# Performance work log

Measured on AMD Instinct MI355X. Metric: run time of the kernel, lower is better.

## Reference

```python
import jax, jax.numpy as jnp
import numpy as np

VAR_FLOOR = 0.002
BS, A, IN, H, L, NNH, ATT, NACT = 1024, 32, 96, 64, 16, 64, 32, 16


def _lin(x, w, b):
    return x @ w.T + b


def _lrelu(x):
    return jax.nn.leaky_relu(x, 0.01)


def setup_inputs() -> dict:
    key = jax.random.key(0)
    ks = jax.random.split(key, 24)
    def w(k, o, i):
        return jax.random.normal(k, (o, i), jnp.float32) / np.float32(np.sqrt(i))
    def b(k, o):
        return jax.random.normal(k, (o,), jnp.float32) * 0.01
    N = BS * A
    return {
        "inputs": jax.random.normal(ks[0], (N, IN), jnp.float32),
        "hidden_state": jax.random.normal(ks[1], (N, H), jnp.float32),
        "eps": jax.random.normal(ks[2], (N, A * L), jnp.float32),
        "fc1_w": w(ks[3], H, IN), "fc1_b": b(ks[4], H),
        "gru_wih": w(ks[5], 3 * H, H), "gru_whh": w(ks[6], 3 * H, H),
        "gru_bih": b(ks[7], 3 * H), "gru_bhh": b(ks[8], 3 * H),
        "fc2_w": w(ks[9], NACT, H), "fc2_b": b(ks[10], NACT),
        "emb_w1": w(ks[11], NNH, H), "emb_b1": b(ks[12], NNH),
        "bn_g": jnp.ones((NNH,), jnp.float32), "bn_b": jnp.zeros((NNH,), jnp.float32),
        "emb_w2": w(ks[13], A * L * 2, NNH), "emb_b2": b(ks[14], A * L * 2),
        "msg_w1": w(ks[15], NNH, H + L), "msg_b1": b(ks[16], NNH),
        "msg_w2": w(ks[17], NACT, NNH), "msg_b2": b(ks[18], NACT),
        "wq_w": w(ks[19], ATT, H), "wq_b": b(ks[20], ATT),
        "wk_w": w(ks[21], ATT, L), "wk_b": b(ks[22], ATT),
        "bs": BS, "t": 0,
    }


def reference(inputs, hidden_state, eps, fc1_w, fc1_b, gru_wih, gru_whh, gru_bih,
              gru_bhh, fc2_w, fc2_b, emb_w1, emb_b1, bn_g, bn_b, emb_w2, emb_b2,
              msg_w1, msg_b1, msg_w2, msg_b2, wq_w, wq_b, wk_w, wk_b, bs, t):
    Hd = fc1_w.shape[0]
    x = jax.nn.relu(_lin(inputs, fc1_w, fc1_b))
    h_in = hidden_state.reshape(-1, Hd)
    # GRUCell
    gi = _lin(x, gru_wih, gru_bih)
    gh = _lin(h_in, gru_whh, gru_bhh)
    ir, iz, inn = jnp.split(gi, 3, axis=-1)
    hr, hz, hn = jnp.split(gh, 3, axis=-1)
    r = jax.nn.sigmoid(ir + hr)
    z = jax.nn.sigmoid(iz + hz)
    n = jnp.tanh(inn + r * hn)
    h = (1.0 - z) * n + z * h_in
    q = _lin(h, fc2_w, fc2_b)
    # embed_net: Linear -> BatchNorm(train) -> LeakyReLU -> Linear
    z1 = _lin(h, emb_w1, emb_b1)
    z1 = bn_g * (z1 - z1.mean(0)) / jnp.sqrt(z1.var(0) + 1e-5) + bn_b
    lat_par = _lin(_lrelu(z1), emb_w2, emb_b2)
    D = lat_par.shape[-1] // 2
    Ld = wk_w.shape[1]
    Ag = D // Ld
    mu = lat_par[:, :D]
    var = jnp.clip(jnp.exp(lat_par[:, D:]), VAR_FLOOR, None)
    latent = (mu + jnp.sqrt(var) * eps).reshape(bs, Ag, Ag, Ld)  # [b,i,j,L]
    # msg_net on (h of receiver j, latent[b,i,j])
    h3 = h.reshape(bs, Ag, Hd)
    h_rep = jnp.broadcast_to(h3[:, None, :, :], (bs, Ag, Ag, Hd))  # [b,i,j]=h[b,j]
    msg_in = jnp.concatenate([h_rep, latent], axis=-1)
    msg = _lin(_lrelu(_lin(msg_in, msg_w1, msg_b1)), msg_w2, msg_b2)  # (b,A,A,n_act)
    # attention gating
    att = wq_w.shape[0]
    query = _lin(h, wq_w, wq_b).reshape(bs, Ag, att) / np.float32(np.sqrt(att))
    key_ = _lin(latent, wk_w, wk_b)  # (b,A,A,att)
    alpha = jnp.einsum('bia,bija->bij', query, key_)
    alpha = jnp.where(jnp.eye(Ag, dtype=bool)[None], -1e9, alpha)
    alpha = jax.nn.softmax(alpha, axis=-1)
    agg = jnp.einsum('bij,bijn->bjn', alpha, msg)  # sum gated msgs over sender i
    return_q = q + agg.reshape(bs * Ag, -1)
    return (return_q, h)
```

## Files before the change

kernel.cpp:

```cpp
#include <hip/hip_runtime.h>
#include <math.h>

namespace {

constexpr int NROW = 32768;
constexpr int HDIM = 64;
constexpr int DH   = 512;

typedef __attribute__((ext_vector_type(8))) short bf16x8;
typedef __attribute__((ext_vector_type(4))) float f32x4;
typedef __attribute__((ext_vector_type(4))) unsigned uint4e;
typedef __attribute__((ext_vector_type(2))) unsigned uint2e;

__device__ __forceinline__ float sigmoidf_(float x) { return 1.f / (1.f + __expf(-x)); }
__device__ __forceinline__ float lrelu_(float x) { return x > 0.f ? x : 0.01f * x; }
__device__ __forceinline__ unsigned pkbf(float a, float b) {
  unsigned ua = __float_as_uint(a) + 0x8000u;
  unsigned ub = __float_as_uint(b) + 0x8000u;
  return __builtin_amdgcn_perm(ub, ua, 0x07060302);
}

__global__ __launch_bounds__(512, 1) void k_fgru(
    const float* __restrict__ in,
    const float* __restrict__ hprev,
    const float* __restrict__ fc1w, const float* __restrict__ fc1b,
    const float* __restrict__ wih, const float* __restrict__ whh,
    const float* __restrict__ bih, const float* __restrict__ bhh,
    float* __restrict__ hT, float* __restrict__ hout) {
  __shared__ char smem[73728];
  const int t = threadIdx.x;
  const int n0 = blockIdx.x * 128;
  short*    xS = (short*)smem;
  unsigned* gU = (unsigned*)(smem + 18432);
  float*    trF = (float*)(smem + 18432);

  const float2* wih2 = (const float2*)wih;
  const float2* whh2 = (const float2*)whh;
  {
    float2 wv[12];
#pragma unroll
    for (int i = 0; i < 12; ++i) {
      int idx = t + 512 * i;
      int row = idx >> 5, kp = idx & 31;
      wv[i] = wih2[row * 32 + kp];
    }
#pragma unroll
    for (int i = 0; i < 12; ++i) {
      int idx = t + 512 * i;
      int row = idx >> 5, kp = idx & 31;
      int gate = row >> 6, cl = row & 63;
      gU[(gate * 64 + cl) * 36 + kp] = pkbf(wv[i].x, wv[i].y);
    }
#pragma unroll
    for (int i = 0; i < 12; ++i) {
      int idx = t + 512 * i;
      int row = idx >> 5, kp = idx & 31;
      wv[i] = whh2[row * 32 + kp];
    }
#pragma unroll
    for (int i = 0; i < 12; ++i) {
      int idx = t + 512 * i;
      int row = idx >> 5, kp = idx & 31;
      int gate = row >> 6, cl = row & 63;
      gU[((gate + 3) * 64 + cl) * 36 + kp] = pkbf(wv[i].x, wv[i].y);
    }
  }

  const int w = t >> 6, l = t & 63;
  const int m = l & 15, g = l >> 4;
  const int rowA = n0 + w * 16 + m;

  bf16x8 af[3];
#pragma unroll
  for (int ks = 0; ks < 3; ++ks) {
    const float4* p = (const float4*)(in + (size_t)rowA * 96 + ks * 32 + g * 8);
    float4 a = p[0], b = p[1];
    union { unsigned u[4]; bf16x8 h; } tw;
    tw.u[0] = pkbf(a.x, a.y); tw.u[1] = pkbf(a.z, a.w);
    tw.u[2] = pkbf(b.x, b.y); tw.u[3] = pkbf(b.z, b.w);
    af[ks] = tw.h;
  }
  {
    f32x4 accx[4];
#pragma unroll
    for (int ct = 0; ct < 4; ++ct) accx[ct] = (f32x4){0.f, 0.f, 0.f, 0.f};
#pragma unroll
    for (int ct = 0; ct < 4; ++ct)
#pragma unroll
      for (int ks = 0; ks < 3; ++ks) {
        const float4* p = (const float4*)(fc1w + (ct * 16 + m) * 96 + ks * 32 + g * 8);
        float4 a = p[0], b = p[1];
        union { unsigned u[4]; bf16x8 h; } tw;
        tw.u[0] = pkbf(a.x, a.y); tw.u[1] = pkbf(a.z, a.w);
        tw.u[2] = pkbf(b.x, b.y); tw.u[3] = pkbf(b.z, b.w);
        accx[ct] = __builtin_amdgcn_mfma_f32_16x16x32_bf16(af[ks], tw.h, accx[ct], 0, 0, 0);
      }
#pragma unroll
    for (int ct = 0; ct < 4; ++ct) {
      int c = ct * 16 + m;
      float bc = fc1b[c];
#pragma unroll
      for (int reg = 0; reg < 4; ++reg) {
        int nl = w * 16 + g * 4 + reg;
        float v = fmaxf(accx[ct][reg] + bc, 0.f);
        xS[nl * 72 + c] = (short)((__float_as_uint(v) + 0x8000u) >> 16);
      }
    }
  }
  __syncthreads();

  bf16x8 ax[2], ah[2];
#pragma unroll
  for (int ks = 0; ks < 2; ++ks) {
    ax[ks] = *(const bf16x8*)(xS + (w * 16 + m) * 72 + ks * 32 + g * 8);
    const float4* p = (const float4*)(hprev + (size_t)rowA * 64 + ks * 32 + g * 8);
    float4 a = p[0], b = p[1];
    union { unsigned u[4]; bf16x8 h; } tw;
    tw.u[0] = pkbf(a.x, a.y); tw.u[1] = pkbf(a.z, a.w);
    tw.u[2] = pkbf(b.x, b.y); tw.u[3] = pkbf(b.z, b.w);
    ah[ks] = tw.h;
  }
  const short* gS = (const short*)gU;
  float hc[4][4];
#pragma unroll 1
  for (int ct = 0; ct < 4; ++ct) {
    f32x4 a_ir = (f32x4){0.f,0.f,0.f,0.f}, a_iz = (f32x4){0.f,0.f,0.f,0.f},
          a_in = (f32x4){0.f,0.f,0.f,0.f}, a_hr = (f32x4){0.f,0.f,0.f,0.f},
          a_hz = (f32x4){0.f,0.f,0.f,0.f}, a_hn = (f32x4){0.f,0.f,0.f,0.f};
    int crow = ct * 16 + m;
#pragma unroll
    for (int ks = 0; ks < 2; ++ks) {
      bf16x8 b0 = *(const bf16x8*)(gS + (0 * 64 + crow) * 72 + ks * 32 + g * 8);
      bf16x8 b1 = *(const bf16x8*)(gS + (1 * 64 + crow) * 72 + ks * 32 + g * 8);
      bf16x8 b2 = *(const bf16x8*)(gS + (2 * 64 + crow) * 72 + ks * 32 + g * 8);
      bf16x8 b3 = *(const bf16x8*)(gS + (3 * 64 + crow) * 72 + ks * 32 + g * 8);
      bf16x8 b4 = *(const bf16x8*)(gS + (4 * 64 + crow) * 72 + ks * 32 + g * 8);
      bf16x8 b5 = *(const bf16x8*)(gS + (5 * 64 + crow) * 72 + ks * 32 + g * 8);
      a_ir = __builtin_amdgcn_mfma_f32_16x16x32_bf16(ax[ks], b0, a_ir, 0, 0, 0);
      a_iz = __builtin_amdgcn_mfma_f32_16x16x32_bf16(ax[ks], b1, a_iz, 0, 0, 0);
      a_in = __builtin_amdgcn_mfma_f32_16x16x32_bf16(ax[ks], b2, a_in, 0, 0, 0);
      a_hr = __builtin_amdgcn_mfma_f32_16x16x32_bf16(ah[ks], b3, a_hr, 0, 0, 0);
      a_hz = __builtin_amdgcn_mfma_f32_16x16x32_bf16(ah[ks], b4, a_hz, 0, 0, 0);
      a_hn = __builtin_amdgcn_mfma_f32_16x16x32_bf16(ah[ks], b5, a_hn, 0, 0, 0);
    }
    float bir = bih[crow], biz = bih[64 + crow], bin = bih[128 + crow];
    float bhr = bhh[crow], bhz = bhh[64 + crow], bhn = bhh[128 + crow];
#pragma unroll
    for (int reg = 0; reg < 4; ++reg) {
      int nl = w * 16 + g * 4 + reg;
      float hv = hprev[(size_t)(n0 + nl) * 64 + crow];
      float r  = sigmoidf_(a_ir[reg] + bir + a_hr[reg] + bhr);
      float z  = sigmoidf_(a_iz[reg] + biz + a_hz[reg] + bhz);
      float nn = tanhf(a_in[reg] + bin + r * (a_hn[reg] + bhn));
      hc[ct][reg] = (1.f - z) * nn + z * hv;
    }
  }
  __syncthreads();
#pragma unroll
  for (int ct = 0; ct < 4; ++ct)
#pragma unroll
    for (int reg = 0; reg < 4; ++reg)
      trF[(ct * 16 + m) * 133 + w * 16 + g * 4 + reg] = hc[ct][reg];
  __syncthreads();
#pragma unroll
  for (int i = 0; i < 16; ++i) {
    int idx = t + 512 * i;
    int nl = idx & 127, cl = idx >> 7;
    hT[(size_t)cl * NROW + n0 + nl] = trF[cl * 133 + nl];
  }
#pragma unroll
  for (int i = 0; i < 16; ++i) {
    int idx = t + 512 * i;
    int c = idx & 63, nl = idx >> 6;
    hout[(size_t)(n0 + nl) * 64 + c] = trF[c * 133 + nl];
  }
}

__global__ __launch_bounds__(256) void k_heads(const float* __restrict__ hT,
    const float* __restrict__ fc2w, const float* __restrict__ fc2b,
    const float* __restrict__ wqw, const float* __restrict__ wkw,
    const float* __restrict__ ew1, const float* __restrict__ eb1,
    float* __restrict__ qT, float* __restrict__ qkT, float* __restrict__ z1T,
    float* __restrict__ part) {
  __shared__ char smem[36864];
  const int t = threadIdx.x;
  const int n0 = blockIdx.x * 128;
  unsigned* hU = (unsigned*)smem;
  unsigned* wU = (unsigned*)(smem + 18432);
  float* sp1 = (float*)(smem + 18432 + 13824);
  float* sp2 = sp1 + 256;
  const float qs = 0.17677669529663687f;

  {
    float va[16], vb[16];
#pragma unroll
    for (int i = 0; i < 16; ++i) {
      int idx = t + 256 * i;
      int nl = idx & 127, kp = idx >> 7;
      va[i] = hT[(size_t)(2 * kp) * NROW + n0 + nl];
      vb[i] = hT[(size_t)(2 * kp + 1) * NROW + n0 + nl];
    }
#pragma unroll
    for (int i = 0; i < 16; ++i) {
      int idx = t + 256 * i;
      int nl = idx & 127, kp = idx >> 7;
      hU[nl * 36 + kp] = pkbf(va[i], vb[i]);
    }
  }
  {
    float2 wv[10];
#pragma unroll
    for (int i = 0; i < 10; ++i) {
      int idx = t + 256 * i;
      int kp = idx & 31, cl = idx >> 5;
      const float* src = (cl < 16) ? (fc2w + cl * 64) : (ew1 + (cl - 16) * 64);
      wv[i] = *(const float2*)(src + 2 * kp);
    }
#pragma unroll
    for (int i = 0; i < 10; ++i) {
      int idx = t + 256 * i;
      int kp = idx & 31, cl = idx >> 5;
      int dst = (cl < 16) ? cl : (cl + 16);
      wU[dst * 36 + kp] = pkbf(wv[i].x, wv[i].y);
    }
  }
  {
    int kp = t & 31, ll = t >> 5;
#pragma unroll
    for (int h = 0; h < 2; ++h) {
      int row = ll + 8 * h;
      float s0 = 0.f, s1 = 0.f;
#pragma unroll
      for (int a = 0; a < 32; ++a) {
        float wk = wkw[a * 16 + row];
        s0 = fmaf(wk, wqw[a * 64 + 2 * kp], s0);
        s1 = fmaf(wk, wqw[a * 64 + 2 * kp + 1], s1);
      }
      wU[(16 + row) * 36 + kp] = pkbf(s0 * qs, s1 * qs);
    }
  }
  __syncthreads();

  const int w = t >> 6, l = t & 63;
  const int m = l & 15, g = l >> 4;
  const short* sH = (const short*)hU;
  const short* sW = (const short*)wU;

  bf16x8 af[2][2];
#pragma unroll
  for (int mt = 0; mt < 2; ++mt)
#pragma unroll
    for (int ks = 0; ks < 2; ++ks)
      af[mt][ks] = *(const bf16x8*)(sH + (w * 32 + mt * 16 + m) * 72 + ks * 32 + g * 8);

  f32x4 acc[2][6];
#pragma unroll
  for (int mt = 0; mt < 2; ++mt)
#pragma unroll
    for (int ct = 0; ct < 6; ++ct) acc[mt][ct] = (f32x4){0.f, 0.f, 0.f, 0.f};
#pragma unroll
  for (int ct = 0; ct < 6; ++ct)
#pragma unroll
    for (int ks = 0; ks < 2; ++ks) {
      bf16x8 bw = *(const bf16x8*)(sW + (ct * 16 + m) * 72 + ks * 32 + g * 8);
#pragma unroll
      for (int mt = 0; mt < 2; ++mt)
        acc[mt][ct] = __builtin_amdgcn_mfma_f32_16x16x32_bf16(af[mt][ks], bw, acc[mt][ct], 0, 0, 0);
    }

  float s1[4], s2[4];
#pragma unroll
  for (int zt = 0; zt < 4; ++zt) { s1[zt] = 0.f; s2[zt] = 0.f; }
#pragma unroll
  for (int mt = 0; mt < 2; ++mt) {
    int nb = n0 + w * 32 + mt * 16 + g * 4;
    {
      float bc = fc2b[m];
      f32x4 v;
#pragma unroll
      for (int reg = 0; reg < 4; ++reg) v[reg] = acc[mt][0][reg] + bc;
      *(f32x4*)(qT + (size_t)m * NROW + nb) = v;
    }
    *(f32x4*)(qkT + (size_t)m * NROW + nb) = acc[mt][1];
#pragma unroll
    for (int ct = 2; ct < 6; ++ct) {
      int z = (ct - 2) * 16 + m;
      float bc = eb1[z];
      f32x4 v;
#pragma unroll
      for (int reg = 0; reg < 4; ++reg) {
        float zv = acc[mt][ct][reg] + bc;
        v[reg] = zv;
        s1[ct - 2] += zv;
        s2[ct - 2] = fmaf(zv, zv, s2[ct - 2]);
      }
      *(f32x4*)(z1T + (size_t)z * NROW + nb) = v;
    }
  }
#pragma unroll
  for (int zt = 0; zt < 4; ++zt) {
    s1[zt] += __shfl_down(s1[zt], 16, 64);
    s1[zt] += __shfl_down(s1[zt], 32, 64);
    s2[zt] += __shfl_down(s2[zt], 16, 64);
    s2[zt] += __shfl_down(s2[zt], 32, 64);
  }
  if (l < 16) {
#pragma unroll
    for (int zt = 0; zt < 4; ++zt) {
      sp1[w * 64 + zt * 16 + m] = s1[zt];
      sp2[w * 64 + zt * 16 + m] = s2[zt];
    }
  }
  __syncthreads();
  if (t < 64) {
    float a1 = sp1[t] + sp1[64 + t] + sp1[128 + t] + sp1[192 + t];
    float a2 = sp2[t] + sp2[64 + t] + sp2[128 + t] + sp2[192 + t];
    part[(size_t)blockIdx.x * 128 + t] = a1;
    part[(size_t)blockIdx.x * 128 + 64 + t] = a2;
  }
}

__global__ void k_bnstat(const float* __restrict__ part,
    const float* __restrict__ bng, const float* __restrict__ bnb,
    float* __restrict__ stat) {
  int c = threadIdx.x;
  float s1 = 0.f, s2 = 0.f;
  for (int b = 0; b < 256; ++b) {
    s1 += part[(size_t)b * 128 + c];
    s2 += part[(size_t)b * 128 + 64 + c];
  }
  float mean = s1 * (1.f / NROW);
  float var = s2 * (1.f / NROW) - mean * mean;
  float rstd = rsqrtf(var + 1e-5f);
  float sc = bng[c] * rstd;
  stat[c] = sc;
  stat[64 + c] = bnb[c] - mean * sc;
}

__global__ __launch_bounds__(512, 1) void k_emb_gemm(const float* __restrict__ z1T,
    const float* __restrict__ stat,
    const float* __restrict__ ew2, const float* __restrict__ eb2,
    const float* __restrict__ eps,
    unsigned* __restrict__ latB16g) {
  __shared__ char smem[161280];
  const int t = threadIdx.x;
  const int n0 = blockIdx.x * 128;
  unsigned* aU = (unsigned*)smem;
  unsigned* wU = (unsigned*)(smem + 17920);

  const int w = t >> 6, l = t & 63;
  const int m = l & 15, g = l >> 4;
  const float2* ew2_2 = (const float2*)ew2;
  const float stdfloor = 0.04472135955f;

  {
    float va[8], vb[8];
#pragma unroll
    for (int i = 0; i < 8; ++i) {
      int idx = t + 512 * i;
      int nl = idx & 127, kp = idx >> 7;
      va[i] = z1T[(size_t)(2 * kp) * NROW + n0 + nl];
      vb[i] = z1T[(size_t)(2 * kp + 1) * NROW + n0 + nl];
    }
#pragma unroll
    for (int i = 0; i < 8; ++i) {
      int idx = t + 512 * i;
      int nl = idx & 127, kp = idx >> 7;
      float v0 = lrelu_(fmaf(stat[2 * kp], va[i], stat[64 + 2 * kp]));
      float v1 = lrelu_(fmaf(stat[2 * kp + 1], vb[i], stat[64 + 2 * kp + 1]));
      aU[nl * 35 + kp] = pkbf(v0, v1);
    }
  }
#pragma unroll 1
  for (int rb = 0; rb < 4; ++rb) {
    float2 wv[16];
#pragma unroll
    for (int j = 0; j < 16; ++j) {
      int idx = t + 512 * (rb * 16 + j);
      int kp = idx & 31, r = idx >> 5;
      wv[j] = ew2_2[(size_t)r * 32 + kp];
    }
#pragma unroll
    for (int j = 0; j < 16; ++j) {
      int idx = t + 512 * (rb * 16 + j);
      int kp = idx & 31, r = idx >> 5;
      int chunk = (r >> 6) & 7;
      int lrow = (r & 63) + ((r >> 9) << 6);
      wU[chunk * 4480 + lrow * 35 + kp] = pkbf(wv[j].x, wv[j].y);
    }
  }
  float epsC[16];
#pragma unroll
  for (int ct = 0; ct < 4; ++ct)
#pragma unroll
    for (int reg = 0; reg < 4; ++reg)
      epsC[ct * 4 + reg] =
          eps[(size_t)(n0 + w * 16 + g * 4 + reg) * 512 + ct * 16 + m];
  __syncthreads();

  const short* sA = (const short*)aU;
  bf16x8 af[2];
#pragma unroll
  for (int ks = 0; ks < 2; ++ks)
    af[ks] = *(const bf16x8*)(sA + (w * 16 + m) * 70 + ks * 32 + g * 8);

  const int rowG = n0 + w * 16 + g * 4;

#pragma unroll 1
  for (int cb = 0; cb < 8; ++cb) {
    const int c0 = cb * 64;
    float epsN[16];
    if (cb < 7) {
#pragma unroll
      for (int ct = 0; ct < 4; ++ct)
#pragma unroll
        for (int reg = 0; reg < 4; ++reg)
          epsN[ct * 4 + reg] =
              eps[(size_t)(rowG + reg) * 512 + c0 + 64 + ct * 16 + m];
    }

    const short* sW = (const short*)(wU + cb * 4480);
    f32x4 accm[4], accl[4];
#pragma unroll
    for (int ct = 0; ct < 4; ++ct) {
      accm[ct] = (f32x4){0.f, 0.f, 0.f, 0.f};
      accl[ct] = (f32x4){0.f, 0.f, 0.f, 0.f};
    }
#pragma unroll
    for (int ct = 0; ct < 4; ++ct)
#pragma unroll
      for (int ks = 0; ks < 2; ++ks) {
        bf16x8 bm = *(const bf16x8*)(sW + (ct * 16 + m) * 70 + ks * 32 + g * 8);
        bf16x8 bl = *(const bf16x8*)(sW + (64 + ct * 16 + m) * 70 + ks * 32 + g * 8);
        accm[ct] = __builtin_amdgcn_mfma_f32_16x16x32_bf16(af[ks], bm, accm[ct], 0, 0, 0);
        accl[ct] = __builtin_amdgcn_mfma_f32_16x16x32_bf16(af[ks], bl, accl[ct], 0, 0, 0);
      }

#pragma unroll
    for (int ct = 0; ct < 4; ++ct) {
      int c = c0 + ct * 16 + m;
      float ebm = eb2[c], ebl = eb2[DH + c];
#pragma unroll
      for (int reg = 0; reg < 4; ++reg) {
        float mu = accm[ct][reg] + ebm;
        float lv = accl[ct][reg] + ebl;
        float sd = fmaxf(__expf(0.5f * lv), stdfloor);
        float lat = fmaf(sd, epsC[ct * 4 + reg], mu);
        float lat2 = __shfl_xor(lat, 1, 64);
        if (!(m & 1)) {
          latB16g[(size_t)(rowG + reg) * 256 + (c0 >> 1) + ct * 8 + (m >> 1)] =
              pkbf(lat, lat2);
        }
      }
    }
#pragma unroll
    for (int i2 = 0; i2 < 16; ++i2) epsC[i2] = epsN[i2];
  }
}

constexpr int LATB_OFF = 0;
constexpr int H3B_OFF  = 40960;
constexpr int W1H_OFF  = 45568;
constexpr int W1L_OFF  = 54784;
constexpr int W2P_OFF  = 57344;
constexpr int ALL_OFF  = 59648;
constexpr int MT_OFF   = 63872;
constexpr int QKL_OFF  = 74112;
__global__ __launch_bounds__(256, 1) void k_msg(
    const unsigned* __restrict__ latB16g, const float* __restrict__ qkT,
    const float* __restrict__ qT, const float* __restrict__ hrow,
    const float* __restrict__ w1, const float* __restrict__ b1,
    const float* __restrict__ w2, const float* __restrict__ b2,
    float* __restrict__ out) {
  __shared__ char smem[76672];
  const int t = threadIdx.x;
  const int b = blockIdx.x;
  const int b32 = b * 32;
  unsigned* latB_dw = (unsigned*)(smem + LATB_OFF);

  {
    const uint4e* g4 = (const uint4e*)latB16g + (size_t)b32 * 64;
#pragma unroll
    for (int half = 0; half < 2; ++half) {
      uint4e v[4];
#pragma unroll
      for (int it = 0; it < 4; ++it) v[it] = g4[t + 256 * (4 * half + it)];
#pragma unroll
      for (int it = 0; it < 4; ++it) {
        int idx = t + 256 * (4 * half + it);
        int i = idx >> 6;
        int rem = idx & 63;
        int j = rem >> 1, hh = rem & 1;
        unsigned* dst = latB_dw + (i * 32 + j) * 10 + hh * 4;
        *(uint2e*)dst = (uint2e){v[it].x, v[it].y};
        *(uint2e*)(dst + 2) = (uint2e){v[it].z, v[it].w};
      }
    }
  }
  {
    float* qkL = (float*)(smem + QKL_OFF);
    int i = t & 31;
    float v0 = qkT[(size_t)((t >> 5)) * NROW + b32 + i];
    float v1 = qkT[(size_t)((t >> 5) + 8) * NROW + b32 + i];
    qkL[i * 20 + (t >> 5)] = v0;
    qkL[i * 20 + (t >> 5) + 8] = v1;
  }
  {
    int cp = t & 31, jj = t >> 5;
    const float2* h2 = (const float2*)hrow;
    float2 hv[4];
#pragma unroll
    for (int it = 0; it < 4; ++it)
      hv[it] = h2[((size_t)(b32 + jj + 8 * it) * 64 + 2 * cp) >> 1];
    unsigned* dst = (unsigned*)(smem + H3B_OFF);
#pragma unroll
    for (int it = 0; it < 4; ++it)
      dst[(jj + 8 * it) * 36 + cp] = pkbf(hv[it].x, hv[it].y);
  }
  {
    int kp = t & 31, cc = t >> 5;
    const float2* w12 = (const float2*)w1;
    float2 wv[8];
#pragma unroll
    for (int it = 0; it < 8; ++it)
      wv[it] = w12[((cc + 8 * it) * 80 + 2 * kp) >> 1];
    unsigned* dst = (unsigned*)(smem + W1H_OFF);
#pragma unroll
    for (int it = 0; it < 8; ++it)
      dst[(cc + 8 * it) * 36 + kp] = pkbf(wv[it].x, wv[it].y);
  }
  {
    int lp = t & 7, cc = t >> 3;
    const float2* w12 = (const float2*)w1;
    float2 wv[2];
#pragma unroll
    for (int it = 0; it < 2; ++it)
      wv[it] = w12[((cc + 32 * it) * 80 + 64 + 2 * lp) >> 1];
    unsigned* dst = (unsigned*)(smem + W1L_OFF);
#pragma unroll
    for (int it = 0; it < 2; ++it)
      dst[(cc + 32 * it) * 10 + lp] = pkbf(wv[it].x, wv[it].y);
  }
  {
    int pp = t & 31, nn = t >> 5;
    const float2* w22 = (const float2*)w2;
    int p = 2 * pp;
    int c = ((p >> 2) & 3) * 16 + (p >> 4) * 4 + (p & 3);
    float2 wv0 = w22[(nn * 64 + c) >> 1];
    float2 wv1 = w22[((nn + 8) * 64 + c) >> 1];
    unsigned* dst = (unsigned*)(smem + W2P_OFF);
    dst[nn * 36 + pp] = pkbf(wv0.x, wv0.y);
    dst[(nn + 8) * 36 + pp] = pkbf(wv1.x, wv1.y);
  }
  __syncthreads();

  {
    const float* qkL = (const float*)(smem + QKL_OFF);
    float* alL = (float*)(smem + ALL_OFF);
#pragma unroll 1
    for (int p = 0; p < 4; ++p) {
      int i = (t >> 5) + 8 * p;
      int j = t & 31;
      const unsigned* lr = latB_dw + (i * 32 + j) * 10;
      float acc = 0.f;
#pragma unroll
      for (int d = 0; d < 8; ++d) {
        unsigned u = lr[d];
        float lo = __uint_as_float(u << 16);
        float hi = __uint_as_float(u & 0xffff0000u);
        acc = fmaf(lo, qkL[i * 20 + 2 * d], acc);
        acc = fmaf(hi, qkL[i * 20 + 2 * d + 1], acc);
      }
      if (j == i) acc = -1e9f;
      float mx = acc;
#pragma unroll
      for (int msk = 16; msk > 0; msk >>= 1) mx = fmaxf(mx, __shfl_xor(mx, msk, 32));
      float e = __expf(acc - mx);
      float s = e;
#pragma unroll
      for (int msk = 16; msk > 0; msk >>= 1) s += __shfl_xor(s, msk, 32);
      alL[i * 33 + j] = e / s;
    }
  }

  const int w = t >> 6, l = t & 63;
  const int n15 = l & 15, q = l >> 4;
  const int jh = w & 1, ibase = (w >> 1) * 16;
  const bool kact = (q < 2);

  f32x4 hp[4];
#pragma unroll
  for (int ct = 0; ct < 4; ++ct) hp[ct] = (f32x4){0.f, 0.f, 0.f, 0.f};
#pragma unroll
  for (int ct = 0; ct < 4; ++ct)
#pragma unroll
    for (int ks = 0; ks < 2; ++ks) {
      bf16x8 aF = *(const bf16x8*)(smem + W1H_OFF + (ct * 16 + n15) * 144 + ks * 64 + q * 16);
      bf16x8 bF = *(const bf16x8*)(smem + H3B_OFF + (jh * 16 + n15) * 144 + ks * 64 + q * 16);
      hp[ct] = __builtin_amdgcn_mfma_f32_16x16x32_bf16(aF, bF, hp[ct], 0, 0, 0);
    }
#pragma unroll
  for (int ct = 0; ct < 4; ++ct)
#pragma unroll
    for (int reg = 0; reg < 4; ++reg)
      hp[ct][reg] += b1[ct * 16 + q * 4 + reg];

  bf16x8 aL[4];
#pragma unroll
  for (int ct = 0; ct < 4; ++ct) {
    union { unsigned u[4]; bf16x8 h; } tmp;
    tmp.u[0] = tmp.u[1] = tmp.u[2] = tmp.u[3] = 0u;
    if (kact) {
      const unsigned* p = (const unsigned*)(smem + W1L_OFF) + (ct * 16 + n15) * 10 + q * 4;
      uint2e d0 = *(const uint2e*)p;
      uint2e d1 = *(const uint2e*)(p + 2);
      tmp.u[0] = d0.x; tmp.u[1] = d0.y; tmp.u[2] = d1.x; tmp.u[3] = d1.y;
    }
    aL[ct] = tmp.h;
  }
  bf16x8 w2F[2];
#pragma unroll
  for (int ks = 0; ks < 2; ++ks)
    w2F[ks] = *(const bf16x8*)(smem + W2P_OFF + n15 * 144 + ks * 64 + q * 16);
  float b2v[4];
#pragma unroll
  for (int reg = 0; reg < 4; ++reg) b2v[reg] = b2[q * 4 + reg];

  __syncthreads();

  float agg[4] = {0.f, 0.f, 0.f, 0.f};
  char* wb = smem + MT_OFF + w * 2560;
  const float* alLf = (const float*)(smem + ALL_OFF);
#pragma unroll 1
  for (int it = 0; it < 16; ++it) {
    int ii = ibase + it;
    int r = ii * 32 + jh * 16 + n15;
    union { unsigned u[4]; bf16x8 h; } latF;
    latF.u[0] = latF.u[1] = latF.u[2] = latF.u[3] = 0u;
    if (kact) {
      const unsigned* p = latB_dw + r * 10 + q * 4;
      uint2e d0 = *(const uint2e*)p;
      uint2e d1 = *(const uint2e*)(p + 2);
      latF.u[0] = d0.x; latF.u[1] = d0.y; latF.u[2] = d1.x; latF.u[3] = d1.y;
    }
    f32x4 acc[4];
#pragma unroll
    for (int ct = 0; ct < 4; ++ct) {
      acc[ct] = (f32x4){0.f, 0.f, 0.f, 0.f};
      acc[ct] = __builtin_amdgcn_mfma_f32_16x16x32_bf16(aL[ct], latF.h, acc[ct], 0, 0, 0);
    }
#pragma unroll
    for (int h = 0; h < 2; ++h) {
      float m0[4], m1[4];
#pragma unroll
      for (int reg = 0; reg < 4; ++reg) {
        float v0 = acc[2 * h][reg] + hp[2 * h][reg];
        float v1 = acc[2 * h + 1][reg] + hp[2 * h + 1][reg];
        m0[reg] = fmaxf(v0, 0.01f * v0);
        m1[reg] = fmaxf(v1, 0.01f * v1);
      }
      uint4e pk4;
      pk4.x = pkbf(m0[0], m0[1]); pk4.y = pkbf(m0[2], m0[3]);
      pk4.z = pkbf(m1[0], m1[1]); pk4.w = pkbf(m1[2], m1[3]);
      int qp = (2 * q + h) & 3;
      *(uint4e*)(wb + (q >> 1) * 1280 + n15 * 80 + qp * 16) = pk4;
    }
    f32x4 msg = (f32x4){0.f, 0.f, 0.f, 0.f};
#pragma unroll
    for (int ks = 0; ks < 2; ++ks) {
      bf16x8 mF = *(const bf16x8*)(wb + ks * 1280 + n15 * 80 + q * 16);
      msg = __builtin_amdgcn_mfma_f32_16x16x32_bf16(w2F[ks], mF, msg, 0, 0, 0);
    }
    float aw = alLf[ii * 33 + jh * 16 + n15];
#pragma unroll
    for (int reg = 0; reg < 4; ++reg)
      agg[reg] = fmaf(aw, msg[reg] + b2v[reg], agg[reg]);
  }
  {
    f32x4 av; av[0] = agg[0]; av[1] = agg[1]; av[2] = agg[2]; av[3] = agg[3];
    *(f32x4*)(wb + n15 * 80 + q * 16) = av;
  }
  __syncthreads();
#pragma unroll
  for (int tt = 0; tt < 2; ++tt) {
    int idx = t + 256 * tt;
    int jg = idx >> 4, nn = idx & 15;
    int jh2 = jg >> 4, jl = jg & 15;
    float a0 = *(const float*)(smem + MT_OFF + jh2 * 2560 + jl * 80 + nn * 4);
    float a1 = *(const float*)(smem + MT_OFF + (jh2 + 2) * 2560 + jl * 80 + nn * 4);
    out[(size_t)b * 512 + idx] = a0 + a1 + qT[(size_t)nn * NROW + b32 + jg];
  }
}

}

extern "C" void kernel_launch(void* const* d_in, const int* in_sizes, int n_in,
                              void* d_out, int out_size, void* d_ws, size_t ws_size,
                              hipStream_t stream) {
  (void)in_sizes; (void)n_in; (void)out_size; (void)ws_size;
  const float* inputs = (const float*)d_in[0];
  const float* hidden = (const float*)d_in[1];
  const float* eps    = (const float*)d_in[2];
  const float* fc1w   = (const float*)d_in[3];
  const float* fc1b   = (const float*)d_in[4];
  const float* wih    = (const float*)d_in[5];
  const float* whh    = (const float*)d_in[6];
  const float* bih    = (const float*)d_in[7];
  const float* bhh    = (const float*)d_in[8];
  const float* fc2w   = (const float*)d_in[9];
  const float* fc2b   = (const float*)d_in[10];
  const float* ew1    = (const float*)d_in[11];
  const float* eb1    = (const float*)d_in[12];
  const float* bng    = (const float*)d_in[13];
  const float* bnb    = (const float*)d_in[14];
  const float* ew2    = (const float*)d_in[15];
  const float* eb2    = (const float*)d_in[16];
  const float* w1     = (const float*)d_in[17];
  const float* b1     = (const float*)d_in[18];
  const float* w2     = (const float*)d_in[19];
  const float* b2     = (const float*)d_in[20];
  const float* wqw    = (const float*)d_in[21];
  const float* wkw    = (const float*)d_in[23];

  float* ws = (float*)d_ws;
  float* hT     = ws;
  float* qT     = ws + 2097152;
  float* qkT    = ws + 2621440;
  float* z1T    = ws + 3670016;
  float* part   = ws + 5767168;
  float* stat   = ws + 5832704;
  unsigned* latB16g = (unsigned*)(ws + 5832832);

  float* out_q = (float*)d_out;
  float* out_h = (float*)d_out + 524288;

  hipLaunchKernelGGL(k_fgru, dim3(256), dim3(512), 0, stream,
                     inputs, hidden, fc1w, fc1b, wih, whh, bih, bhh, hT, out_h);
  hipLaunchKernelGGL(k_heads, dim3(256), dim3(256), 0, stream,
                     hT, fc2w, fc2b, wqw, wkw, ew1, eb1, qT, qkT, z1T, part);
  hipLaunchKernelGGL(k_bnstat, dim3(1), dim3(64), 0, stream, part, bng, bnb, stat);
  hipLaunchKernelGGL(k_emb_gemm, dim3(256), dim3(512), 0, stream, z1T, stat, ew2, eb2, eps, latB16g);
  hipLaunchKernelGGL(k_msg, dim3(1024), dim3(256), 0, stream,
                     latB16g, qkT, qT, out_h, w1, b1, w2, b2, out_q);
}
```

Before: 258.7 us.

## Split emb GEMM over channel halves with triple-buffered weight staging

The embedding GEMM kernel now runs 512 blocks, each covering half of the output channels. Previously each block staged the whole 1024x64 weight matrix in LDS (about 160KB), which allowed only one block per CU. Now each block streams 64-channel weight chunks through three rotating LDS buffers, overlapping global loads and bf16 packing with the MFMA compute, so LDS use falls to about 72KB and more blocks can be resident. The BN stat reduction is also spread over 256 threads with a shared-memory combine, and the LDS row pitch changes from 35 to 36 words to allow vector stores. The cost is that each A tile (z1 rows) is now loaded and normalized twice, once per half.

```diff
diff --git a/kernel.cpp b/kernel.cpp
--- a/kernel.cpp
+++ b/kernel.cpp
@@ -320,38 +320,79 @@
   }
 }
 
-__global__ void k_bnstat(const float* __restrict__ part,
+__global__ __launch_bounds__(256) void k_bnstat(const float* __restrict__ part,
     const float* __restrict__ bng, const float* __restrict__ bnb,
     float* __restrict__ stat) {
-  int c = threadIdx.x;
+  __shared__ float red[512];
+  const int t = threadIdx.x;
+  const int c = t & 63, q = t >> 6;
   float s1 = 0.f, s2 = 0.f;
-  for (int b = 0; b < 256; ++b) {
+#pragma unroll 4
+  for (int b = q; b < 256; b += 4) {
     s1 += part[(size_t)b * 128 + c];
     s2 += part[(size_t)b * 128 + 64 + c];
   }
-  float mean = s1 * (1.f / NROW);
-  float var = s2 * (1.f / NROW) - mean * mean;
-  float rstd = rsqrtf(var + 1e-5f);
-  float sc = bng[c] * rstd;
-  stat[c] = sc;
-  stat[64 + c] = bnb[c] - mean * sc;
+  red[q * 64 + c] = s1;
+  red[256 + q * 64 + c] = s2;
+  __syncthreads();
+  if (t < 64) {
+    float a1 = red[t] + red[64 + t] + red[128 + t] + red[192 + t];
+    float a2 = red[256 + t] + red[320 + t] + red[384 + t] + red[448 + t];
+    float mean = a1 * (1.f / NROW);
+    float var = a2 * (1.f / NROW) - mean * mean;
+    float rstd = rsqrtf(var + 1e-5f);
+    float sc = bng[t] * rstd;
+    stat[t] = sc;
+    stat[64 + t] = bnb[t] - mean * sc;
+  }
 }
 
-__global__ __launch_bounds__(512, 1) void k_emb_gemm(const float* __restrict__ z1T,
+__global__ __launch_bounds__(512, 4) void k_emb_gemm(const float* __restrict__ z1T,
     const float* __restrict__ stat,
     const float* __restrict__ ew2, const float* __restrict__ eb2,
     const float* __restrict__ eps,
     unsigned* __restrict__ latB16g) {
-  __shared__ char smem[161280];
+  __shared__ char smem[73728];
   const int t = threadIdx.x;
-  const int n0 = blockIdx.x * 128;
+  const int nb = blockIdx.x >> 1;
+  const int half = blockIdx.x & 1;
+  const int n0 = nb * 128;
+  const int ch0 = half * 256;
+
   unsigned* aU = (unsigned*)smem;
-  unsigned* wU = (unsigned*)(smem + 17920);
+  unsigned* wB0 = (unsigned*)(smem + 18432);
+  unsigned* wB1 = (unsigned*)(smem + 36864);
+  unsigned* wB2 = (unsigned*)(smem + 55296);
 
   const int w = t >> 6, l = t & 63;
   const int m = l & 15, g = l >> 4;
-  const float2* ew2_2 = (const float2*)ew2;
+  const float4* ew2_4 = (const float4*)ew2;
   const float stdfloor = 0.04472135955f;
+  const int rowG = n0 + w * 16 + g * 4;
+  const int kp4 = t & 15, cl = t >> 4;
+
+  float4 wmA, wmB, wlA, wlB;
+  float epsC[16], epsN[16], epsT[16];
+
+  auto loadW = [&](int c2) {
+    wmA = ew2_4[(size_t)(c2 + cl) * 16 + kp4];
+    wmB = ew2_4[(size_t)(c2 + 32 + cl) * 16 + kp4];
+    wlA = ew2_4[(size_t)(512 + c2 + cl) * 16 + kp4];
+    wlB = ew2_4[(size_t)(512 + c2 + 32 + cl) * 16 + kp4];
+  };
+  auto packW = [&](unsigned* bp) {
+    *(uint2e*)(bp + cl * 36 + kp4 * 2) = (uint2e){pkbf(wmA.x, wmA.y), pkbf(wmA.z, wmA.w)};
+    *(uint2e*)(bp + (32 + cl) * 36 + kp4 * 2) = (uint2e){pkbf(wmB.x, wmB.y), pkbf(wmB.z, wmB.w)};
+    *(uint2e*)(bp + (64 + cl) * 36 + kp4 * 2) = (uint2e){pkbf(wlA.x, wlA.y), pkbf(wlA.z, wlA.w)};
+    *(uint2e*)(bp + (96 + cl) * 36 + kp4 * 2) = (uint2e){pkbf(wlB.x, wlB.y), pkbf(wlB.z, wlB.w)};
+  };
+  auto loadE = [&](int c0v, float* arr) {
+#pragma unroll
+    for (int ct = 0; ct < 4; ++ct)
+#pragma unroll
+      for (int reg = 0; reg < 4; ++reg)
+        arr[ct * 4 + reg] = eps[(size_t)(rowG + reg) * 512 + c0v + ct * 16 + m];
+  };
 
   {
     float va[8], vb[8];
@@ -368,58 +409,24 @@
       int nl = idx & 127, kp = idx >> 7;
       float v0 = lrelu_(fmaf(stat[2 * kp], va[i], stat[64 + 2 * kp]));
       float v1 = lrelu_(fmaf(stat[2 * kp + 1], vb[i], stat[64 + 2 * kp + 1]));
-      aU[nl * 35 + kp] = pkbf(v0, v1);
-    }
-  }
-#pragma unroll 1
-  for (int rb = 0; rb < 4; ++rb) {
-    float2 wv[16];
-#pragma unroll
-    for (int j = 0; j < 16; ++j) {
-      int idx = t + 512 * (rb * 16 + j);
-      int kp = idx & 31, r = idx >> 5;
-      wv[j] = ew2_2[(size_t)r * 32 + kp];
-    }
-#pragma unroll
-    for (int j = 0; j < 16; ++j) {
-      int idx = t + 512 * (rb * 16 + j);
-      int kp = idx & 31, r = idx >> 5;
-      int chunk = (r >> 6) & 7;
-      int lrow = (r & 63) + ((r >> 9) << 6);
-      wU[chunk * 4480 + lrow * 35 + kp] = pkbf(wv[j].x, wv[j].y);
-    }
-  }
-  float epsC[16];
-#pragma unroll
-  for (int ct = 0; ct < 4; ++ct)
-#pragma unroll
-    for (int reg = 0; reg < 4; ++reg)
-      epsC[ct * 4 + reg] =
-          eps[(size_t)(n0 + w * 16 + g * 4 + reg) * 512 + ct * 16 + m];
+      aU[nl * 36 + kp] = pkbf(v0, v1);
+    }
+  }
+  loadW(ch0);
+  packW(wB0);
+  loadW(ch0 + 64);
+  loadE(ch0, epsC);
+  loadE(ch0 + 64, epsN);
   __syncthreads();
 
   const short* sA = (const short*)aU;
   bf16x8 af[2];
 #pragma unroll
   for (int ks = 0; ks < 2; ++ks)
-    af[ks] = *(const bf16x8*)(sA + (w * 16 + m) * 70 + ks * 32 + g * 8);
-
-  const int rowG = n0 + w * 16 + g * 4;
-
-#pragma unroll 1
-  for (int cb = 0; cb < 8; ++cb) {
-    const int c0 = cb * 64;
-    float epsN[16];
-    if (cb < 7) {
-#pragma unroll
-      for (int ct = 0; ct < 4; ++ct)
-#pragma unroll
-        for (int reg = 0; reg < 4; ++reg)
-          epsN[ct * 4 + reg] =
-              eps[(size_t)(rowG + reg) * 512 + c0 + 64 + ct * 16 + m];
-    }
-
-    const short* sW = (const short*)(wU + cb * 4480);
+    af[ks] = *(const bf16x8*)(sA + (w * 16 + m) * 72 + ks * 32 + g * 8);
+
+  auto compute = [&](const unsigned* wbu, int c0, const float* epsArr) {
+    const short* sW = (const short*)wbu;
     f32x4 accm[4], accl[4];
 #pragma unroll
     for (int ct = 0; ct < 4; ++ct) {
@@ -430,12 +437,11 @@
     for (int ct = 0; ct < 4; ++ct)
 #pragma unroll
       for (int ks = 0; ks < 2; ++ks) {
-        bf16x8 bm = *(const bf16x8*)(sW + (ct * 16 + m) * 70 + ks * 32 + g * 8);
-        bf16x8 bl = *(const bf16x8*)(sW + (64 + ct * 16 + m) * 70 + ks * 32 + g * 8);
+        bf16x8 bm = *(const bf16x8*)(sW + (ct * 16 + m) * 72 + ks * 32 + g * 8);
+        bf16x8 bl = *(const bf16x8*)(sW + (64 + ct * 16 + m) * 72 + ks * 32 + g * 8);
         accm[ct] = __builtin_amdgcn_mfma_f32_16x16x32_bf16(af[ks], bm, accm[ct], 0, 0, 0);
         accl[ct] = __builtin_amdgcn_mfma_f32_16x16x32_bf16(af[ks], bl, accl[ct], 0, 0, 0);
       }
-
 #pragma unroll
     for (int ct = 0; ct < 4; ++ct) {
       int c = c0 + ct * 16 + m;
@@ -445,7 +451,7 @@
         float mu = accm[ct][reg] + ebm;
         float lv = accl[ct][reg] + ebl;
         float sd = fmaxf(__expf(0.5f * lv), stdfloor);
-        float lat = fmaf(sd, epsC[ct * 4 + reg], mu);
+        float lat = fmaf(sd, epsArr[ct * 4 + reg], mu);
         float lat2 = __shfl_xor(lat, 1, 64);
         if (!(m & 1)) {
           latB16g[(size_t)(rowG + reg) * 256 + (c0 >> 1) + ct * 8 + (m >> 1)] =
@@ -453,9 +459,28 @@
         }
       }
     }
-#pragma unroll
-    for (int i2 = 0; i2 < 16; ++i2) epsC[i2] = epsN[i2];
-  }
+  };
+
+  packW(wB1);
+  __syncthreads();
+  loadW(ch0 + 128);
+  loadE(ch0 + 128, epsT);
+  compute(wB0, ch0, epsC);
+#pragma unroll
+  for (int i = 0; i < 16; ++i) { epsC[i] = epsN[i]; epsN[i] = epsT[i]; }
+  packW(wB2);
+  __syncthreads();
+  loadW(ch0 + 192);
+  loadE(ch0 + 192, epsT);
+  compute(wB1, ch0 + 64, epsC);
+#pragma unroll
+  for (int i = 0; i < 16; ++i) { epsC[i] = epsN[i]; epsN[i] = epsT[i]; }
+  packW(wB0);
+  __syncthreads();
+  compute(wB2, ch0 + 128, epsC);
+#pragma unroll
+  for (int i = 0; i < 16; ++i) epsC[i] = epsN[i];
+  compute(wB0, ch0 + 192, epsC);
 }
 
 constexpr int LATB_OFF = 0;
@@ -738,8 +763,8 @@
                      inputs, hidden, fc1w, fc1b, wih, whh, bih, bhh, hT, out_h);
   hipLaunchKernelGGL(k_heads, dim3(256), dim3(256), 0, stream,
                      hT, fc2w, fc2b, wqw, wkw, ew1, eb1, qT, qkT, z1T, part);
-  hipLaunchKernelGGL(k_bnstat, dim3(1), dim3(64), 0, stream, part, bng, bnb, stat);
-  hipLaunchKernelGGL(k_emb_gemm, dim3(256), dim3(512), 0, stream, z1T, stat, ew2, eb2, eps, latB16g);
+  hipLaunchKernelGGL(k_bnstat, dim3(1), dim3(256), 0, stream, part, bng, bnb, stat);
+  hipLaunchKernelGGL(k_emb_gemm, dim3(512), dim3(512), 0, stream, z1T, stat, ew2, eb2, eps, latB16g);
   hipLaunchKernelGGL(k_msg, dim3(1024), dim3(256), 0, stream,
                      latB16g, qkT, qT, out_h, w1, b1, w2, b2, out_q);
 }
```

After: 256.8 us. Within noise of the previous version (-0.7%).
